# Performance work log

Measured on AMD Instinct MI355X. Metric: run time of the kernel, lower is better.

## Reference

```python
import jax, jax.numpy as jnp
import numpy as np

K = 16          # nsample (ball-query neighbors via topk smallest sqdist)
EPS = 1e-5      # BatchNorm eps


def conv1(x, W, b):
    # pointwise Conv1d (kernel=1): x [B,N,Cin], W [Cout,Cin], b [Cout] -> [B,N,Cout]
    return jnp.einsum('bnc,oc->bno', x, W) + b


def bn_train(x, gamma, beta):
    # BatchNorm1d in training mode: stats over batch and length dims
    mean = jnp.mean(x, axis=(0, 1))
    var = jnp.var(x, axis=(0, 1))
    return (x - mean) * jax.lax.rsqrt(var + EPS) * gamma + beta


def farthest_point_sample(xyz, npoint):
    # xyz [B,N,3] -> idx [B,npoint]; deterministic start at index 0
    B, N, _ = xyz.shape

    def step(carry, _):
        dist, far = carry                                        # [B,N], [B]
        centroid = jnp.take_along_axis(xyz, far[:, None, None], axis=1)  # [B,1,3]
        d = jnp.sum((xyz - centroid) ** 2, axis=-1)              # [B,N]
        dist = jnp.minimum(dist, d)
        nxt = jnp.argmax(dist, axis=1).astype(jnp.int32)
        return (dist, nxt), far

    init = (jnp.full((B, N), jnp.finfo(xyz.dtype).max, xyz.dtype),
            jnp.zeros((B,), jnp.int32))
    _, idx = jax.lax.scan(step, init, None, length=npoint)       # [npoint,B]
    return idx.T                                                  # [B,npoint]


def sqdist(a, b):
    # a [B,S,3], b [B,N,3] -> [B,S,N]
    return (jnp.sum(a ** 2, -1)[:, :, None]
            + jnp.sum(b ** 2, -1)[:, None, :]
            - 2.0 * jnp.einsum('bsc,bnc->bsn', a, b))


def gather_groups(pc, idx):
    # pc [B,N,D], idx [B,S,K] -> [B,S,K,D]
    return jax.vmap(lambda p, i: p[i])(pc, idx)


def setup_inputs() -> dict:
    key = jax.random.key(0)
    ks = jax.random.split(key, 8)
    B, N = 8, 4096
    mid, out, cin = 32, 64, 3
    s = lambda fan: 1.0 / np.sqrt(fan)
    return {
        'x_in': jax.random.normal(ks[0], (B, N, cin), jnp.float32),
        'W1': jax.random.normal(ks[1], (mid, cin), jnp.float32) * s(cin),
        'b1': jnp.zeros((mid,), jnp.float32),
        'g1': jnp.ones((mid,), jnp.float32),
        'be1': jnp.zeros((mid,), jnp.float32),
        'W2': jax.random.normal(ks[2], (out, mid), jnp.float32) * s(mid),
        'b2': jnp.zeros((out,), jnp.float32),
        'W3': jax.random.normal(ks[3], (out, out + cin), jnp.float32) * s(out + cin),
        'b3': jnp.zeros((out,), jnp.float32),
        'g2': jnp.ones((out,), jnp.float32),
        'be2': jnp.zeros((out,), jnp.float32),
        'W4': jax.random.normal(ks[4], (out, out), jnp.float32) * s(out),
        'b4': jnp.zeros((out,), jnp.float32),
    }


def reference(x_in, W1, b1, g1, be1, W2, b2, W3, b3, g2, be2, W4, b4):
    B, N, C = x_in.shape
    S = N // 2
    # first_mlp: Conv1d -> BN -> ReLU -> Conv1d (all pointwise)
    h = jax.nn.relu(bn_train(conv1(x_in, W1, b1), g1, be1))
    feats = conv1(h, W2, b2)                                  # [B,N,64]
    # sample_and_group(npoint=N//2, nsample=K, xyz=x_in, points=feats)
    fps_idx = farthest_point_sample(x_in, S)                  # [B,S]
    new_xyz = jnp.take_along_axis(x_in, fps_idx[..., None], axis=1)  # [B,S,3]
    d = sqdist(new_xyz, x_in)                                 # [B,S,N]
    _, idx = jax.lax.top_k(-d, K)                             # [B,S,K] smallest dists
    grouped_xyz = gather_groups(x_in, idx) - new_xyz[:, :, None, :]  # [B,S,K,3]
    grouped_pts = gather_groups(feats, idx)                   # [B,S,K,64]
    x_cat = jnp.concatenate([grouped_xyz, grouped_pts], axis=-1)  # [B,S,K,67]
    pooled = jnp.max(x_cat, axis=2)                           # [B,S,67]
    # last_mlp
    h = jax.nn.relu(bn_train(conv1(pooled, W3, b3), g2, be2))
    return conv1(h, W4, b4)                                   # [B,S,64]
```

## Files before the change

### kernel.cpp

```cpp
#include <hip/hip_runtime.h>
#include <float.h>

#define BB   8
#define NN   4096
#define SS   2048
#define KK   16
#define MID  32
#define COUT 64
#define CAT  67
#define M1   (BB*NN)
#define M2   (BB*SS)
#define EPSB 1e-5f

#define WS_CTR   0
#define WS_RED1  16
#define WS_RED2  640
#define WS_FPS   1024
#define WS_FEATS (1024 + 16384)
#define WS_POOL  (WS_FEATS + M1*COUT)

struct SA  { float red[8][9]; };
struct SB4 { float4 Pc[NN]; alignas(16) unsigned long long sv[2][8]; };
struct SB3 { float W1s[96]; float abv[64]; float W2s[2048]; float b2s[64]; float mom[9]; };
struct SC  { float4 Pq[NN]; unsigned candd[64][129]; unsigned candi[64][129]; int fin[64][16]; };
struct SC2 { float W3s[64 * CAT]; float b3s[64]; float ps[128]; };
struct SE  { float W3t[CAT * 64]; float W4s[4096]; float b3s[64]; float b4s[64]; float ab[128]; };
union  SU  { SA a; SB4 b4; SB3 b3; SC c; SC2 c2; SE e; };

__device__ __forceinline__ unsigned long long u64max(unsigned long long a,
                                                     unsigned long long b) {
    return a > b ? a : b;
}

template <int CTRL>
__device__ __forceinline__ unsigned long long dpp_swap_max(unsigned long long v) {
    int lo = (int)(unsigned)v;
    int hi = (int)(unsigned)(v >> 32);
    int olo = __builtin_amdgcn_update_dpp(0, lo, CTRL, 0xF, 0xF, false);
    int ohi = __builtin_amdgcn_update_dpp(0, hi, CTRL, 0xF, 0xF, false);
    unsigned long long ov = ((unsigned long long)(unsigned)ohi << 32) | (unsigned)olo;
    return u64max(v, ov);
}

__device__ __forceinline__ void barrier_join(int* ctr, int target) {
    __syncthreads();
    if (threadIdx.x == 0) {
        __threadfence();
        atomicAdd(ctr, 1);
        while (atomicAdd(ctr, 0) < target) __builtin_amdgcn_s_sleep(16);
        __threadfence();
    }
    __syncthreads();
}

__global__ __launch_bounds__(512) void fused(
        const float* __restrict__ xin,
        const float* __restrict__ W1, const float* __restrict__ b1,
        const float* __restrict__ g1, const float* __restrict__ be1,
        const float* __restrict__ W2, const float* __restrict__ b2,
        const float* __restrict__ W3, const float* __restrict__ b3,
        const float* __restrict__ g2, const float* __restrict__ be2,
        const float* __restrict__ W4, const float* __restrict__ b4,
        float* __restrict__ ws, float* __restrict__ out) {
    __shared__ SU sm;
    int blk = blockIdx.x, tid = threadIdx.x;
    int* ctr = (int*)ws;
    (void)b1;

    if (blk >= 8) {
        if (blk < 72) {
            int p = (blk - 8) * 512 + tid;
            float x0 = xin[3 * p], x1 = xin[3 * p + 1], x2 = xin[3 * p + 2];
            float r[9];
            r[0] = x0; r[1] = x1; r[2] = x2;
            r[3] = x0 * x0; r[4] = x0 * x1; r[5] = x0 * x2;
            r[6] = x1 * x1; r[7] = x1 * x2; r[8] = x2 * x2;
#pragma unroll
            for (int m = 32; m; m >>= 1) {
#pragma unroll
                for (int q = 0; q < 9; q++) r[q] += __shfl_down(r[q], m, 64);
            }
            if ((tid & 63) == 0) {
#pragma unroll
                for (int q = 0; q < 9; q++) sm.a.red[tid >> 6][q] = r[q];
            }
            __syncthreads();
            if (tid == 0) {
#pragma unroll
                for (int q = 0; q < 9; q++) {
                    float s = 0.f;
#pragma unroll
                    for (int w = 0; w < 8; w++) s += sm.a.red[w][q];
                    ws[WS_RED1 + (blk - 8) * 9 + q] = s;
                }
            }
        }
        barrier_join(ctr + 0, 248);
    }

    if (blk < 8) {
        int b = blk;
        const float* xb = xin + (size_t)b * NN * 3;
        float px[8], py[8], pz[8], dist[8];
#pragma unroll
        for (int k = 0; k < 8; k++) {
            int i = tid + (k << 9);
            float x = xb[3 * i], y = xb[3 * i + 1], z = xb[3 * i + 2];
            px[k] = x; py[k] = y; pz[k] = z; dist[k] = FLT_MAX;
            sm.b4.Pc[i] = make_float4(x, y, z, 0.f);
        }
        int* fidx = (int*)(ws + WS_FPS) + b * SS;
        if (tid == 0) fidx[0] = 0;
        __syncthreads();
        float4 c0 = sm.b4.Pc[0];
        float cx = c0.x, cy = c0.y, cz = c0.z;
        int wid = tid >> 6, lane = tid & 63;
        for (int t = 1; t < SS; t++) {
            float bv = -1.f; int bi = 0;
#pragma unroll
            for (int k = 0; k < 8; k++) {
                float dx = px[k] - cx, dy = py[k] - cy, dz = pz[k] - cz;
                float d = fmaf(dz, dz, fmaf(dy, dy, dx * dx));
                float nd = fminf(dist[k], d);
                dist[k] = nd;
                bool bt = nd > bv;
                bv = bt ? nd : bv; bi = bt ? (tid + (k << 9)) : bi;
            }
            unsigned long long v =
                ((unsigned long long)__float_as_uint(bv) << 32) | (unsigned)(~bi);
            v = dpp_swap_max<0xB1>(v);
            v = dpp_swap_max<0x4E>(v);
            v = dpp_swap_max<0x141>(v);
            v = dpp_swap_max<0x140>(v);
            {
                int a16 = ((lane ^ 16) << 2), a32 = ((lane ^ 32) << 2), a48 = ((lane ^ 48) << 2);
                int lo = (int)(unsigned)v, hi = (int)(unsigned)(v >> 32);
                int lo16 = __builtin_amdgcn_ds_bpermute(a16, lo);
                int hi16 = __builtin_amdgcn_ds_bpermute(a16, hi);
                int lo32 = __builtin_amdgcn_ds_bpermute(a32, lo);
                int hi32 = __builtin_amdgcn_ds_bpermute(a32, hi);
                int lo48 = __builtin_amdgcn_ds_bpermute(a48, lo);
                int hi48 = __builtin_amdgcn_ds_bpermute(a48, hi);
                unsigned long long v16 = ((unsigned long long)(unsigned)hi16 << 32) | (unsigned)lo16;
                unsigned long long v32 = ((unsigned long long)(unsigned)hi32 << 32) | (unsigned)lo32;
                unsigned long long v48 = ((unsigned long long)(unsigned)hi48 << 32) | (unsigned)lo48;
                v = u64max(u64max(v, v16), u64max(v32, v48));
            }
            int par = t & 1;
            if (lane == 0) sm.b4.sv[par][wid] = v;
            __syncthreads();
            const ulonglong2* sp = (const ulonglong2*)sm.b4.sv[par];
            ulonglong2 q0 = sp[0], q1 = sp[1], q2 = sp[2], q3 = sp[3];
            unsigned long long m0 = u64max(q0.x, q0.y), m1 = u64max(q1.x, q1.y);
            unsigned long long m2 = u64max(q2.x, q2.y), m3 = u64max(q3.x, q3.y);
            unsigned long long best = u64max(u64max(m0, m1), u64max(m2, m3));
            int bsel = (int)(~(unsigned)best);
            float4 cc = sm.b4.Pc[bsel];
            cx = cc.x; cy = cc.y; cz = cc.z;
            if (tid == 0) fidx[t] = bsel;
        }
    } else if (blk < 72) {
        for (int j = tid; j < 96; j += 512) sm.b3.W1s[j] = W1[j];
        if (tid < 64) sm.b3.b2s[tid] = b2[tid];
        for (int j = tid; j < 2048; j += 512) sm.b3.W2s[j] = W2[j];
        if (tid < 9) {
            float s = 0.f;
            for (int k = 0; k < 64; k++) s += ws[WS_RED1 + k * 9 + tid];
            sm.b3.mom[tid] = s;
        }
        __syncthreads();
        if (tid < MID) {
            float S0 = sm.b3.mom[0], S1 = sm.b3.mom[1], S2 = sm.b3.mom[2];
            float C00 = sm.b3.mom[3], C01 = sm.b3.mom[4], C02 = sm.b3.mom[5];
            float C11 = sm.b3.mom[6], C12 = sm.b3.mom[7], C22 = sm.b3.mom[8];
            float w0 = W1[3 * tid], w1 = W1[3 * tid + 1], w2 = W1[3 * tid + 2];
            float invM = 1.f / (float)M1;
            float meanc = (w0 * S0 + w1 * S1 + w2 * S2) * invM;
            float wCw = w0 * w0 * C00 + w1 * w1 * C11 + w2 * w2 * C22 +
                        2.f * (w0 * w1 * C01 + w0 * w2 * C02 + w1 * w2 * C12);
            float var = wCw * invM - meanc * meanc;
            float a = g1[tid] * rsqrtf(var + EPSB);
            sm.b3.abv[tid] = a;
            sm.b3.abv[MID + tid] = be1[tid] - meanc * a;
        }
        __syncthreads();
        int p = (blk - 8) * 512 + tid;
        float x0 = xin[3 * p], x1 = xin[3 * p + 1], x2 = xin[3 * p + 2];
        float h[MID];
#pragma unroll
        for (int o = 0; o < MID; o++) {
            float y = fmaf(sm.b3.W1s[3 * o + 2], x2,
                     fmaf(sm.b3.W1s[3 * o + 1], x1, sm.b3.W1s[3 * o] * x0));
            h[o] = fmaxf(0.f, fmaf(sm.b3.abv[o], y, sm.b3.abv[MID + o]));
        }
        float* fo = ws + WS_FEATS + (size_t)p * COUT;
#pragma unroll
        for (int j = 0; j < COUT; j += 4) {
            float a0 = sm.b3.b2s[j], a1v = sm.b3.b2s[j + 1];
            float a2v = sm.b3.b2s[j + 2], a3v = sm.b3.b2s[j + 3];
#pragma unroll
            for (int o = 0; o < MID; o++) {
                float hv = h[o];
                a0  = fmaf(sm.b3.W2s[(j)     * MID + o], hv, a0);
                a1v = fmaf(sm.b3.W2s[(j + 1) * MID + o], hv, a1v);
                a2v = fmaf(sm.b3.W2s[(j + 2) * MID + o], hv, a2v);
                a3v = fmaf(sm.b3.W2s[(j + 3) * MID + o], hv, a3v);
            }
            *(float4*)(fo + j) = make_float4(a0, a1v, a2v, a3v);
        }
    }
    barrier_join(ctr + 1, 256);

    {
        int b = blk >> 5;
        const float* xb = xin + (size_t)b * NN * 3;
        for (int j = tid; j < NN; j += 512) {
            float x = xb[3 * j], y = xb[3 * j + 1], z = xb[3 * j + 2];
            sm.c.Pq[j] = make_float4(x, y, z, (x * x + y * y) + z * z);
        }
        __syncthreads();
        int cl = tid >> 3, q = tid & 7;
        int sg = blk * 64 + cl;
        const int* fidx = (const int*)(ws + WS_FPS);
        int ci = fidx[sg];
        float4 c = sm.c.Pq[ci];
        float an = c.w;
        unsigned long long cv[16];
#pragma unroll
        for (int j = 0; j < 16; j++) cv[j] = ~0ULL;
        unsigned long long cmaxv = ~0ULL; int cpos = 0;
        for (int n0 = 0; n0 < 512; n0++) {
            int n = (q << 9) + ((n0 + q) & 511);
            float4 qq = sm.c.Pq[n];
            float dot = fmaf(c.z, qq.z, fmaf(c.y, qq.y, c.x * qq.x));
            float dd = (an + qq.w) - 2.f * dot;
            unsigned db = __float_as_uint(dd);
            db ^= (unsigned)(((int)db >> 31) | 0x80000000u);
            unsigned long long newv = ((unsigned long long)db << 32) | (unsigned)n;
            if (newv < cmaxv) {
#pragma unroll
                for (int j = 0; j < 16; j++) cv[j] = (j == cpos) ? newv : cv[j];
                unsigned long long m1a[8]; int p1a[8];
#pragma unroll
                for (int j = 0; j < 8; j++) {
                    bool s = cv[2 * j + 1] > cv[2 * j];
                    m1a[j] = s ? cv[2 * j + 1] : cv[2 * j];
                    p1a[j] = s ? 2 * j + 1 : 2 * j;
                }
                unsigned long long m2a[4]; int p2a[4];
#pragma unroll
                for (int j = 0; j < 4; j++) {
                    bool s = m1a[2 * j + 1] > m1a[2 * j];
                    m2a[j] = s ? m1a[2 * j + 1] : m1a[2 * j];
                    p2a[j] = s ? p1a[2 * j + 1] : p1a[2 * j];
                }
                unsigned long long m3a, m3b; int p3a, p3b;
                { bool s = m2a[1] > m2a[0]; m3a = s ? m2a[1] : m2a[0]; p3a = s ? p2a[1] : p2a[0]; }
                { bool s = m2a[3] > m2a[2]; m3b = s ? m2a[3] : m2a[2]; p3b = s ? p2a[3] : p2a[2]; }
                bool s = m3b > m3a;
                cmaxv = s ? m3b : m3a; cpos = s ? p3b : p3a;
            }
        }
#pragma unroll
        for (int j = 0; j < 16; j++) {
            sm.c.candd[cl][q * 16 + j] = (unsigned)(cv[j] >> 32);
            sm.c.candi[cl][q * 16 + j] = (unsigned)cv[j];
        }
        __syncthreads();
        if (tid < 64) {
            unsigned long long mv[16];
#pragma unroll
            for (int j = 0; j < 16; j++) mv[j] = ~0ULL;
            unsigned long long mx = ~0ULL; int mp = 0;
            for (int k = 0; k < 128; k++) {
                unsigned long long e =
                    ((unsigned long long)sm.c.candd[tid][k] << 32) | sm.c.candi[tid][k];
                if (e < mx) {
#pragma unroll
                    for (int j = 0; j < 16; j++) mv[j] = (j == mp) ? e : mv[j];
                    unsigned long long m1a[8]; int p1a[8];
#pragma unroll
                    for (int j = 0; j < 8; j++) {
                        bool s = mv[2 * j + 1] > mv[2 * j];
                        m1a[j] = s ? mv[2 * j + 1] : mv[2 * j];
                        p1a[j] = s ? 2 * j + 1 : 2 * j;
                    }
                    unsigned long long m2a[4]; int p2a[4];
#pragma unroll
                    for (int j = 0; j < 4; j++) {
                        bool s = m1a[2 * j + 1] > m1a[2 * j];
                        m2a[j] = s ? m1a[2 * j + 1] : m1a[2 * j];
                        p2a[j] = s ? p1a[2 * j + 1] : p1a[2 * j];
                    }
                    unsigned long long m3a, m3b; int p3a, p3b;
                    { bool s = m2a[1] > m2a[0]; m3a = s ? m2a[1] : m2a[0]; p3a = s ? p2a[1] : p2a[0]; }
                    { bool s = m2a[3] > m2a[2]; m3b = s ? m2a[3] : m2a[2]; p3b = s ? p2a[3] : p2a[2]; }
                    bool s = m3b > m3a;
                    mx = s ? m3b : m3a; mp = s ? p3b : p3a;
                }
            }
#pragma unroll
            for (int j = 0; j < 16; j++) sm.c.fin[tid][j] = (int)(unsigned)mv[j];
        }
        __syncthreads();
        int idxs[16];
#pragma unroll
        for (int j = 0; j < 16; j++) idxs[j] = sm.c.fin[cl][j];
        const float* feats = ws + WS_FEATS + (size_t)b * NN * COUT;
        float4 acc0 = make_float4(-FLT_MAX, -FLT_MAX, -FLT_MAX, -FLT_MAX);
        float4 acc1 = acc0;
#pragma unroll 4
        for (int k = 0; k < 16; k++) {
            const float4* fp = (const float4*)(feats + (size_t)idxs[k] * COUT) + q * 2;
            float4 v0 = fp[0], v1 = fp[1];
            acc0.x = fmaxf(acc0.x, v0.x); acc0.y = fmaxf(acc0.y, v0.y);
            acc0.z = fmaxf(acc0.z, v0.z); acc0.w = fmaxf(acc0.w, v0.w);
            acc1.x = fmaxf(acc1.x, v1.x); acc1.y = fmaxf(acc1.y, v1.y);
            acc1.z = fmaxf(acc1.z, v1.z); acc1.w = fmaxf(acc1.w, v1.w);
        }
        float* po = ws + WS_POOL + (size_t)sg * CAT + 3 + q * 8;
        po[0] = acc0.x; po[1] = acc0.y; po[2] = acc0.z; po[3] = acc0.w;
        po[4] = acc1.x; po[5] = acc1.y; po[6] = acc1.z; po[7] = acc1.w;
        if (q == 0) {
            float rx = -FLT_MAX, ry = -FLT_MAX, rz = -FLT_MAX;
#pragma unroll
            for (int k = 0; k < 16; k++) {
                float4 p = sm.c.Pq[idxs[k]];
                rx = fmaxf(rx, p.x - c.x); ry = fmaxf(ry, p.y - c.y); rz = fmaxf(rz, p.z - c.z);
            }
            float* pb = ws + WS_POOL + (size_t)sg * CAT;
            pb[0] = rx; pb[1] = ry; pb[2] = rz;
        }
    }
    barrier_join(ctr + 2, 256);

    if (blk < 64) {
        for (int j = tid; j < 64 * CAT; j += 512) sm.c2.W3s[j] = W3[j];
        if (tid < 64) sm.c2.b3s[tid] = b3[tid];
        if (tid < 128) sm.c2.ps[tid] = 0.f;
        __syncthreads();
        int cch = tid & 63, g = tid >> 6;
        float sum = 0.f, sq = 0.f;
        for (int m = 0; m < 32; m++) {
            int row = blk * 256 + g * 32 + m;
            const float* r = ws + WS_POOL + (size_t)row * CAT;
            float y = sm.c2.b3s[cch];
            for (int j = 0; j < CAT; j++) y = fmaf(sm.c2.W3s[cch * CAT + j], r[j], y);
            sum += y; sq = fmaf(y, y, sq);
        }
        atomicAdd(&sm.c2.ps[cch], sum);
        atomicAdd(&sm.c2.ps[64 + cch], sq);
        __syncthreads();
        if (tid < 128) atomicAdd(ws + WS_RED2 + tid, sm.c2.ps[tid]);
    }
    barrier_join(ctr + 3, 256);

    if (blk < 32) {
        for (int lin = tid; lin < CAT * 64; lin += 512) {
            int j = lin >> 6, o = lin & 63;
            sm.e.W3t[lin] = W3[o * CAT + j];
        }
        for (int j = tid; j < 4096; j += 512) sm.e.W4s[j] = W4[j];
        if (tid < 64) {
            sm.e.b3s[tid] = b3[tid]; sm.e.b4s[tid] = b4[tid];
            float inv = 1.f / (float)M2;
            float mean = ws[WS_RED2 + tid] * inv;
            float var = ws[WS_RED2 + 64 + tid] * inv - mean * mean;
            float a = g2[tid] * rsqrtf(var + EPSB);
            sm.e.ab[tid] = a;
            sm.e.ab[64 + tid] = be2[tid] - mean * a;
        }
        __syncthreads();
        int pt = blk * 512 + tid;
        const float* row = ws + WS_POOL + (size_t)pt * CAT;
        float h[64];
#pragma unroll
        for (int c = 0; c < 64; c++) h[c] = sm.e.b3s[c];
        for (int j = 0; j < CAT; j++) {
            float pj = row[j];
#pragma unroll
            for (int c = 0; c < 64; c++) h[c] = fmaf(sm.e.W3t[j * 64 + c], pj, h[c]);
        }
#pragma unroll
        for (int c = 0; c < 64; c++) h[c] = fmaxf(0.f, fmaf(sm.e.ab[c], h[c], sm.e.ab[64 + c]));
        float* op = out + (size_t)pt * 64;
        for (int o = 0; o < 64; o += 4) {
            float a0 = sm.e.b4s[o], a1v = sm.e.b4s[o + 1];
            float a2v = sm.e.b4s[o + 2], a3v = sm.e.b4s[o + 3];
#pragma unroll
            for (int c = 0; c < 64; c++) {
                float hv = h[c];
                a0  = fmaf(sm.e.W4s[(o)     * 64 + c], hv, a0);
                a1v = fmaf(sm.e.W4s[(o + 1) * 64 + c], hv, a1v);
                a2v = fmaf(sm.e.W4s[(o + 2) * 64 + c], hv, a2v);
                a3v = fmaf(sm.e.W4s[(o + 3) * 64 + c], hv, a3v);
            }
            *(float4*)(op + o) = make_float4(a0, a1v, a2v, a3v);
        }
    }
}

extern "C" void kernel_launch(void* const* d_in, const int* in_sizes, int n_in,
                              void* d_out, int out_size, void* d_ws, size_t ws_size,
                              hipStream_t stream) {
    (void)in_sizes; (void)n_in; (void)out_size; (void)ws_size;
    const float* xin = (const float*)d_in[0];
    const float* W1  = (const float*)d_in[1];
    const float* b1  = (const float*)d_in[2];
    const float* g1  = (const float*)d_in[3];
    const float* be1 = (const float*)d_in[4];
    const float* W2  = (const float*)d_in[5];
    const float* b2  = (const float*)d_in[6];
    const float* W3  = (const float*)d_in[7];
    const float* b3  = (const float*)d_in[8];
    const float* g2  = (const float*)d_in[9];
    const float* be2 = (const float*)d_in[10];
    const float* W4  = (const float*)d_in[11];
    const float* b4  = (const float*)d_in[12];
    float* ws  = (float*)d_ws;
    float* out = (float*)d_out;

    hipMemsetAsync(d_ws, 0, 4096, stream);
    void* args[] = {
        (void*)&xin, (void*)&W1, (void*)&b1, (void*)&g1, (void*)&be1,
        (void*)&W2, (void*)&b2, (void*)&W3, (void*)&b3, (void*)&g2,
        (void*)&be2, (void*)&W4, (void*)&b4, (void*)&ws, (void*)&out
    };
    hipLaunchCooperativeKernel((const void*)fused, dim3(256), dim3(512),
                               args, 0, stream);
}
```

Baseline: 2.361 ms.

## Overlap kNN grouping with FPS via progress flags and dynamic chunk tickets

The farthest-point-sampling blocks now publish their progress every 32 sampled points with release stores. The other 248 blocks compute the first MLP and then pull (batch, chunk) tickets from an atomic counter, spin until that chunk's FPS indices exist, and run top-16 neighbor search and pooling for it. This replaces the old scheme where grouping waited for the whole FPS to finish. The final MLP stages are also spread over all 256 blocks instead of 64 and 32. The cost is spin-wait traffic, reloading the point cloud when a block's batch changes, and the FPS blocks sharing the GPU with the concurrent work.

```diff
diff --git a/kernel.cpp b/kernel.cpp
--- a/kernel.cpp
+++ b/kernel.cpp
@@ -4,17 +4,20 @@
 #define BB   8
 #define NN   4096
 #define SS   2048
-#define KK   16
 #define MID  32
 #define COUT 64
 #define CAT  67
 #define M1   (BB*NN)
 #define M2   (BB*SS)
 #define EPSB 1e-5f
-
-#define WS_CTR   0
-#define WS_RED1  16
-#define WS_RED2  640
+#define NCHUNK 64
+#define CSZ    32
+
+#define WI_CTR   0
+#define WI_TKT   4
+#define WI_PROG  8
+#define WS_RED2  32
+#define WS_RED1  160
 #define WS_FPS   1024
 #define WS_FEATS (1024 + 16384)
 #define WS_POOL  (WS_FEATS + M1*COUT)
@@ -22,7 +25,7 @@
 struct SA  { float red[8][9]; };
 struct SB4 { float4 Pc[NN]; alignas(16) unsigned long long sv[2][8]; };
 struct SB3 { float W1s[96]; float abv[64]; float W2s[2048]; float b2s[64]; float mom[9]; };
-struct SC  { float4 Pq[NN]; unsigned candd[64][129]; unsigned candi[64][129]; int fin[64][16]; };
+struct SC  { float4 Pq[NN]; unsigned long long cand[CSZ][257]; int fin[CSZ][16]; int tkt; };
 struct SC2 { float W3s[64 * CAT]; float b3s[64]; float ps[128]; };
 struct SE  { float W3t[CAT * 64]; float W4s[4096]; float b3s[64]; float b4s[64]; float ab[128]; };
 union  SU  { SA a; SB4 b4; SB3 b3; SC c; SC2 c2; SE e; };
@@ -51,6 +54,32 @@
         __threadfence();
     }
     __syncthreads();
+}
+
+__device__ __forceinline__ void top16_insert(unsigned long long* cv,
+                                             unsigned long long newv,
+                                             unsigned long long& cmaxv, int& cpos) {
+#pragma unroll
+    for (int j = 0; j < 16; j++) cv[j] = (j == cpos) ? newv : cv[j];
+    unsigned long long m1a[8]; int p1a[8];
+#pragma unroll
+    for (int j = 0; j < 8; j++) {
+        bool s = cv[2 * j + 1] > cv[2 * j];
+        m1a[j] = s ? cv[2 * j + 1] : cv[2 * j];
+        p1a[j] = s ? 2 * j + 1 : 2 * j;
+    }
+    unsigned long long m2a[4]; int p2a[4];
+#pragma unroll
+    for (int j = 0; j < 4; j++) {
+        bool s = m1a[2 * j + 1] > m1a[2 * j];
+        m2a[j] = s ? m1a[2 * j + 1] : m1a[2 * j];
+        p2a[j] = s ? p1a[2 * j + 1] : p1a[2 * j];
+    }
+    unsigned long long m3a, m3b; int p3a, p3b;
+    { bool s = m2a[1] > m2a[0]; m3a = s ? m2a[1] : m2a[0]; p3a = s ? p2a[1] : p2a[0]; }
+    { bool s = m2a[3] > m2a[2]; m3b = s ? m2a[3] : m2a[2]; p3b = s ? p2a[3] : p2a[2]; }
+    bool s = m3b > m3a;
+    cmaxv = s ? m3b : m3a; cpos = s ? p3b : p3a;
 }
 
 __global__ __launch_bounds__(512) void fused(
@@ -64,39 +93,10 @@
         float* __restrict__ ws, float* __restrict__ out) {
     __shared__ SU sm;
     int blk = blockIdx.x, tid = threadIdx.x;
-    int* ctr = (int*)ws;
+    int* ctri  = (int*)ws;
+    int* prog  = ctri + WI_PROG;
+    int* fidxg = (int*)(ws + WS_FPS);
     (void)b1;
-
-    if (blk >= 8) {
-        if (blk < 72) {
-            int p = (blk - 8) * 512 + tid;
-            float x0 = xin[3 * p], x1 = xin[3 * p + 1], x2 = xin[3 * p + 2];
-            float r[9];
-            r[0] = x0; r[1] = x1; r[2] = x2;
-            r[3] = x0 * x0; r[4] = x0 * x1; r[5] = x0 * x2;
-            r[6] = x1 * x1; r[7] = x1 * x2; r[8] = x2 * x2;
-#pragma unroll
-            for (int m = 32; m; m >>= 1) {
-#pragma unroll
-                for (int q = 0; q < 9; q++) r[q] += __shfl_down(r[q], m, 64);
-            }
-            if ((tid & 63) == 0) {
-#pragma unroll
-                for (int q = 0; q < 9; q++) sm.a.red[tid >> 6][q] = r[q];
-            }
-            __syncthreads();
-            if (tid == 0) {
-#pragma unroll
-                for (int q = 0; q < 9; q++) {
-                    float s = 0.f;
-#pragma unroll
-                    for (int w = 0; w < 8; w++) s += sm.a.red[w][q];
-                    ws[WS_RED1 + (blk - 8) * 9 + q] = s;
-                }
-            }
-        }
-        barrier_join(ctr + 0, 248);
-    }
 
     if (blk < 8) {
         int b = blk;
@@ -109,8 +109,8 @@
             px[k] = x; py[k] = y; pz[k] = z; dist[k] = FLT_MAX;
             sm.b4.Pc[i] = make_float4(x, y, z, 0.f);
         }
-        int* fidx = (int*)(ws + WS_FPS) + b * SS;
-        if (tid == 0) fidx[0] = 0;
+        if (tid == 0)
+            __hip_atomic_store(fidxg + b * SS, 0, __ATOMIC_RELAXED, __HIP_MEMORY_SCOPE_AGENT);
         __syncthreads();
         float4 c0 = sm.b4.Pc[0];
         float cx = c0.x, cy = c0.y, cz = c0.z;
@@ -157,192 +157,192 @@
             int bsel = (int)(~(unsigned)best);
             float4 cc = sm.b4.Pc[bsel];
             cx = cc.x; cy = cc.y; cz = cc.z;
-            if (tid == 0) fidx[t] = bsel;
-        }
-    } else if (blk < 72) {
-        for (int j = tid; j < 96; j += 512) sm.b3.W1s[j] = W1[j];
-        if (tid < 64) sm.b3.b2s[tid] = b2[tid];
-        for (int j = tid; j < 2048; j += 512) sm.b3.W2s[j] = W2[j];
-        if (tid < 9) {
-            float s = 0.f;
-            for (int k = 0; k < 64; k++) s += ws[WS_RED1 + k * 9 + tid];
-            sm.b3.mom[tid] = s;
-        }
-        __syncthreads();
-        if (tid < MID) {
-            float S0 = sm.b3.mom[0], S1 = sm.b3.mom[1], S2 = sm.b3.mom[2];
-            float C00 = sm.b3.mom[3], C01 = sm.b3.mom[4], C02 = sm.b3.mom[5];
-            float C11 = sm.b3.mom[6], C12 = sm.b3.mom[7], C22 = sm.b3.mom[8];
-            float w0 = W1[3 * tid], w1 = W1[3 * tid + 1], w2 = W1[3 * tid + 2];
-            float invM = 1.f / (float)M1;
-            float meanc = (w0 * S0 + w1 * S1 + w2 * S2) * invM;
-            float wCw = w0 * w0 * C00 + w1 * w1 * C11 + w2 * w2 * C22 +
-                        2.f * (w0 * w1 * C01 + w0 * w2 * C02 + w1 * w2 * C12);
-            float var = wCw * invM - meanc * meanc;
-            float a = g1[tid] * rsqrtf(var + EPSB);
-            sm.b3.abv[tid] = a;
-            sm.b3.abv[MID + tid] = be1[tid] - meanc * a;
-        }
-        __syncthreads();
-        int p = (blk - 8) * 512 + tid;
-        float x0 = xin[3 * p], x1 = xin[3 * p + 1], x2 = xin[3 * p + 2];
-        float h[MID];
-#pragma unroll
-        for (int o = 0; o < MID; o++) {
-            float y = fmaf(sm.b3.W1s[3 * o + 2], x2,
-                     fmaf(sm.b3.W1s[3 * o + 1], x1, sm.b3.W1s[3 * o] * x0));
-            h[o] = fmaxf(0.f, fmaf(sm.b3.abv[o], y, sm.b3.abv[MID + o]));
-        }
-        float* fo = ws + WS_FEATS + (size_t)p * COUT;
-#pragma unroll
-        for (int j = 0; j < COUT; j += 4) {
-            float a0 = sm.b3.b2s[j], a1v = sm.b3.b2s[j + 1];
-            float a2v = sm.b3.b2s[j + 2], a3v = sm.b3.b2s[j + 3];
+            if (tid == 0) {
+                __hip_atomic_store(fidxg + b * SS + t, bsel,
+                                   __ATOMIC_RELAXED, __HIP_MEMORY_SCOPE_AGENT);
+                if (((t + 1) & (CSZ - 1)) == 0)
+                    __hip_atomic_store(prog + b, t + 1,
+                                       __ATOMIC_RELEASE, __HIP_MEMORY_SCOPE_AGENT);
+            }
+        }
+        barrier_join(ctri + 2, 256);
+    } else {
+        if (blk < 72) {
+            int p = (blk - 8) * 512 + tid;
+            float x0 = xin[3 * p], x1 = xin[3 * p + 1], x2 = xin[3 * p + 2];
+            float r[9];
+            r[0] = x0; r[1] = x1; r[2] = x2;
+            r[3] = x0 * x0; r[4] = x0 * x1; r[5] = x0 * x2;
+            r[6] = x1 * x1; r[7] = x1 * x2; r[8] = x2 * x2;
+#pragma unroll
+            for (int m = 32; m; m >>= 1) {
+#pragma unroll
+                for (int q = 0; q < 9; q++) r[q] += __shfl_down(r[q], m, 64);
+            }
+            if ((tid & 63) == 0) {
+#pragma unroll
+                for (int q = 0; q < 9; q++) sm.a.red[tid >> 6][q] = r[q];
+            }
+            __syncthreads();
+            if (tid == 0) {
+#pragma unroll
+                for (int q = 0; q < 9; q++) {
+                    float s = 0.f;
+#pragma unroll
+                    for (int w = 0; w < 8; w++) s += sm.a.red[w][q];
+                    ws[WS_RED1 + (blk - 8) * 9 + q] = s;
+                }
+            }
+            barrier_join(ctri + 0, 64);
+            for (int j = tid; j < 96; j += 512) sm.b3.W1s[j] = W1[j];
+            if (tid < 64) sm.b3.b2s[tid] = b2[tid];
+            for (int j = tid; j < 2048; j += 512) sm.b3.W2s[j] = W2[j];
+            if (tid < 9) {
+                float s = 0.f;
+                for (int k = 0; k < 64; k++) s += ws[WS_RED1 + k * 9 + tid];
+                sm.b3.mom[tid] = s;
+            }
+            __syncthreads();
+            if (tid < MID) {
+                float S0 = sm.b3.mom[0], S1 = sm.b3.mom[1], S2 = sm.b3.mom[2];
+                float C00 = sm.b3.mom[3], C01 = sm.b3.mom[4], C02 = sm.b3.mom[5];
+                float C11 = sm.b3.mom[6], C12 = sm.b3.mom[7], C22 = sm.b3.mom[8];
+                float w0 = W1[3 * tid], w1 = W1[3 * tid + 1], w2 = W1[3 * tid + 2];
+                float invM = 1.f / (float)M1;
+                float meanc = (w0 * S0 + w1 * S1 + w2 * S2) * invM;
+                float wCw = w0 * w0 * C00 + w1 * w1 * C11 + w2 * w2 * C22 +
+                            2.f * (w0 * w1 * C01 + w0 * w2 * C02 + w1 * w2 * C12);
+                float var = wCw * invM - meanc * meanc;
+                float a = g1[tid] * rsqrtf(var + EPSB);
+                sm.b3.abv[tid] = a;
+                sm.b3.abv[MID + tid] = be1[tid] - meanc * a;
+            }
+            __syncthreads();
+            int p2 = (blk - 8) * 512 + tid;
+            float y0 = xin[3 * p2], y1 = xin[3 * p2 + 1], y2 = xin[3 * p2 + 2];
+            float h[MID];
 #pragma unroll
             for (int o = 0; o < MID; o++) {
-                float hv = h[o];
-                a0  = fmaf(sm.b3.W2s[(j)     * MID + o], hv, a0);
-                a1v = fmaf(sm.b3.W2s[(j + 1) * MID + o], hv, a1v);
-                a2v = fmaf(sm.b3.W2s[(j + 2) * MID + o], hv, a2v);
-                a3v = fmaf(sm.b3.W2s[(j + 3) * MID + o], hv, a3v);
-            }
-            *(float4*)(fo + j) = make_float4(a0, a1v, a2v, a3v);
-        }
-    }
-    barrier_join(ctr + 1, 256);
+                float y = fmaf(sm.b3.W1s[3 * o + 2], y2,
+                         fmaf(sm.b3.W1s[3 * o + 1], y1, sm.b3.W1s[3 * o] * y0));
+                h[o] = fmaxf(0.f, fmaf(sm.b3.abv[o], y, sm.b3.abv[MID + o]));
+            }
+            float* fo = ws + WS_FEATS + (size_t)p2 * COUT;
+#pragma unroll
+            for (int j = 0; j < COUT; j += 4) {
+                float a0 = sm.b3.b2s[j], a1v = sm.b3.b2s[j + 1];
+                float a2v = sm.b3.b2s[j + 2], a3v = sm.b3.b2s[j + 3];
+#pragma unroll
+                for (int o = 0; o < MID; o++) {
+                    float hv = h[o];
+                    a0  = fmaf(sm.b3.W2s[(j)     * MID + o], hv, a0);
+                    a1v = fmaf(sm.b3.W2s[(j + 1) * MID + o], hv, a1v);
+                    a2v = fmaf(sm.b3.W2s[(j + 2) * MID + o], hv, a2v);
+                    a3v = fmaf(sm.b3.W2s[(j + 3) * MID + o], hv, a3v);
+                }
+                *(float4*)(fo + j) = make_float4(a0, a1v, a2v, a3v);
+            }
+        }
+        barrier_join(ctri + 1, 248);
+
+        int curb = -1;
+        for (;;) {
+            if (tid == 0) sm.c.tkt = atomicAdd(ctri + WI_TKT, 1);
+            __syncthreads();
+            int tk = sm.c.tkt;
+            if (tk >= BB * NCHUNK) break;
+            int b = tk & 7, c = tk >> 3;
+            if (b != curb) {
+                const float* xb = xin + (size_t)b * NN * 3;
+                for (int j = tid; j < NN; j += 512) {
+                    float x = xb[3 * j], y = xb[3 * j + 1], z = xb[3 * j + 2];
+                    sm.c.Pq[j] = make_float4(x, y, z, (x * x + y * y) + z * z);
+                }
+                curb = b;
+            }
+            if (tid == 0) {
+                int need = (c + 1) * CSZ;
+                while (__hip_atomic_load(prog + b, __ATOMIC_ACQUIRE,
+                                         __HIP_MEMORY_SCOPE_AGENT) < need)
+                    __builtin_amdgcn_s_sleep(8);
+            }
+            __syncthreads();
+            int cc = tid >> 4, q = tid & 15;
+            int s = c * CSZ + cc;
+            int sg = b * SS + s;
+            int ci = __hip_atomic_load(fidxg + sg, __ATOMIC_RELAXED,
+                                       __HIP_MEMORY_SCOPE_AGENT);
+            float4 cen = sm.c.Pq[ci];
+            float an = cen.w;
+            unsigned long long cv[16];
+#pragma unroll
+            for (int j = 0; j < 16; j++) cv[j] = ~0ULL;
+            unsigned long long cmaxv = ~0ULL; int cpos = 0;
+            for (int n0 = 0; n0 < 256; n0++) {
+                int n = (q << 8) + ((n0 + q) & 255);
+                float4 qq = sm.c.Pq[n];
+                float dot = fmaf(cen.z, qq.z, fmaf(cen.y, qq.y, cen.x * qq.x));
+                float dd = (an + qq.w) - 2.f * dot;
+                unsigned db = __float_as_uint(dd);
+                db ^= (unsigned)(((int)db >> 31) | 0x80000000u);
+                unsigned long long newv = ((unsigned long long)db << 32) | (unsigned)n;
+                if (newv < cmaxv) top16_insert(cv, newv, cmaxv, cpos);
+            }
+#pragma unroll
+            for (int j = 0; j < 16; j++) sm.c.cand[cc][q * 16 + j] = cv[j];
+            __syncthreads();
+            if (tid < CSZ) {
+                unsigned long long mv[16];
+#pragma unroll
+                for (int j = 0; j < 16; j++) mv[j] = ~0ULL;
+                unsigned long long mx = ~0ULL; int mp = 0;
+                for (int k = 0; k < 256; k++) {
+                    unsigned long long e = sm.c.cand[tid][k];
+                    if (e < mx) top16_insert(mv, e, mx, mp);
+                }
+#pragma unroll
+                for (int j = 0; j < 16; j++) sm.c.fin[tid][j] = (int)(unsigned)mv[j];
+            }
+            __syncthreads();
+            int idxs[16];
+#pragma unroll
+            for (int j = 0; j < 16; j++) idxs[j] = sm.c.fin[cc][j];
+            const float* feats = ws + WS_FEATS + (size_t)b * NN * COUT;
+            float4 acc = make_float4(-FLT_MAX, -FLT_MAX, -FLT_MAX, -FLT_MAX);
+#pragma unroll 4
+            for (int k = 0; k < 16; k++) {
+                const float4* fp = (const float4*)(feats + (size_t)idxs[k] * COUT) + q;
+                float4 v0 = fp[0];
+                acc.x = fmaxf(acc.x, v0.x); acc.y = fmaxf(acc.y, v0.y);
+                acc.z = fmaxf(acc.z, v0.z); acc.w = fmaxf(acc.w, v0.w);
+            }
+            float* po = ws + WS_POOL + (size_t)sg * CAT;
+            po[3 + q * 4] = acc.x; po[4 + q * 4] = acc.y;
+            po[5 + q * 4] = acc.z; po[6 + q * 4] = acc.w;
+            if (q == 0) {
+                float rx = -FLT_MAX, ry = -FLT_MAX, rz = -FLT_MAX;
+#pragma unroll
+                for (int k = 0; k < 16; k++) {
+                    float4 p = sm.c.Pq[idxs[k]];
+                    rx = fmaxf(rx, p.x - cen.x);
+                    ry = fmaxf(ry, p.y - cen.y);
+                    rz = fmaxf(rz, p.z - cen.z);
+                }
+                po[0] = rx; po[1] = ry; po[2] = rz;
+            }
+        }
+        barrier_join(ctri + 2, 256);
+    }
 
     {
-        int b = blk >> 5;
-        const float* xb = xin + (size_t)b * NN * 3;
-        for (int j = tid; j < NN; j += 512) {
-            float x = xb[3 * j], y = xb[3 * j + 1], z = xb[3 * j + 2];
-            sm.c.Pq[j] = make_float4(x, y, z, (x * x + y * y) + z * z);
-        }
-        __syncthreads();
-        int cl = tid >> 3, q = tid & 7;
-        int sg = blk * 64 + cl;
-        const int* fidx = (const int*)(ws + WS_FPS);
-        int ci = fidx[sg];
-        float4 c = sm.c.Pq[ci];
-        float an = c.w;
-        unsigned long long cv[16];
-#pragma unroll
-        for (int j = 0; j < 16; j++) cv[j] = ~0ULL;
-        unsigned long long cmaxv = ~0ULL; int cpos = 0;
-        for (int n0 = 0; n0 < 512; n0++) {
-            int n = (q << 9) + ((n0 + q) & 511);
-            float4 qq = sm.c.Pq[n];
-            float dot = fmaf(c.z, qq.z, fmaf(c.y, qq.y, c.x * qq.x));
-            float dd = (an + qq.w) - 2.f * dot;
-            unsigned db = __float_as_uint(dd);
-            db ^= (unsigned)(((int)db >> 31) | 0x80000000u);
-            unsigned long long newv = ((unsigned long long)db << 32) | (unsigned)n;
-            if (newv < cmaxv) {
-#pragma unroll
-                for (int j = 0; j < 16; j++) cv[j] = (j == cpos) ? newv : cv[j];
-                unsigned long long m1a[8]; int p1a[8];
-#pragma unroll
-                for (int j = 0; j < 8; j++) {
-                    bool s = cv[2 * j + 1] > cv[2 * j];
-                    m1a[j] = s ? cv[2 * j + 1] : cv[2 * j];
-                    p1a[j] = s ? 2 * j + 1 : 2 * j;
-                }
-                unsigned long long m2a[4]; int p2a[4];
-#pragma unroll
-                for (int j = 0; j < 4; j++) {
-                    bool s = m1a[2 * j + 1] > m1a[2 * j];
-                    m2a[j] = s ? m1a[2 * j + 1] : m1a[2 * j];
-                    p2a[j] = s ? p1a[2 * j + 1] : p1a[2 * j];
-                }
-                unsigned long long m3a, m3b; int p3a, p3b;
-                { bool s = m2a[1] > m2a[0]; m3a = s ? m2a[1] : m2a[0]; p3a = s ? p2a[1] : p2a[0]; }
-                { bool s = m2a[3] > m2a[2]; m3b = s ? m2a[3] : m2a[2]; p3b = s ? p2a[3] : p2a[2]; }
-                bool s = m3b > m3a;
-                cmaxv = s ? m3b : m3a; cpos = s ? p3b : p3a;
-            }
-        }
-#pragma unroll
-        for (int j = 0; j < 16; j++) {
-            sm.c.candd[cl][q * 16 + j] = (unsigned)(cv[j] >> 32);
-            sm.c.candi[cl][q * 16 + j] = (unsigned)cv[j];
-        }
-        __syncthreads();
-        if (tid < 64) {
-            unsigned long long mv[16];
-#pragma unroll
-            for (int j = 0; j < 16; j++) mv[j] = ~0ULL;
-            unsigned long long mx = ~0ULL; int mp = 0;
-            for (int k = 0; k < 128; k++) {
-                unsigned long long e =
-                    ((unsigned long long)sm.c.candd[tid][k] << 32) | sm.c.candi[tid][k];
-                if (e < mx) {
-#pragma unroll
-                    for (int j = 0; j < 16; j++) mv[j] = (j == mp) ? e : mv[j];
-                    unsigned long long m1a[8]; int p1a[8];
-#pragma unroll
-                    for (int j = 0; j < 8; j++) {
-                        bool s = mv[2 * j + 1] > mv[2 * j];
-                        m1a[j] = s ? mv[2 * j + 1] : mv[2 * j];
-                        p1a[j] = s ? 2 * j + 1 : 2 * j;
-                    }
-                    unsigned long long m2a[4]; int p2a[4];
-#pragma unroll
-                    for (int j = 0; j < 4; j++) {
-                        bool s = m1a[2 * j + 1] > m1a[2 * j];
-                        m2a[j] = s ? m1a[2 * j + 1] : m1a[2 * j];
-                        p2a[j] = s ? p1a[2 * j + 1] : p1a[2 * j];
-                    }
-                    unsigned long long m3a, m3b; int p3a, p3b;
-                    { bool s = m2a[1] > m2a[0]; m3a = s ? m2a[1] : m2a[0]; p3a = s ? p2a[1] : p2a[0]; }
-                    { bool s = m2a[3] > m2a[2]; m3b = s ? m2a[3] : m2a[2]; p3b = s ? p2a[3] : p2a[2]; }
-                    bool s = m3b > m3a;
-                    mx = s ? m3b : m3a; mp = s ? p3b : p3a;
-                }
-            }
-#pragma unroll
-            for (int j = 0; j < 16; j++) sm.c.fin[tid][j] = (int)(unsigned)mv[j];
-        }
-        __syncthreads();
-        int idxs[16];
-#pragma unroll
-        for (int j = 0; j < 16; j++) idxs[j] = sm.c.fin[cl][j];
-        const float* feats = ws + WS_FEATS + (size_t)b * NN * COUT;
-        float4 acc0 = make_float4(-FLT_MAX, -FLT_MAX, -FLT_MAX, -FLT_MAX);
-        float4 acc1 = acc0;
-#pragma unroll 4
-        for (int k = 0; k < 16; k++) {
-            const float4* fp = (const float4*)(feats + (size_t)idxs[k] * COUT) + q * 2;
-            float4 v0 = fp[0], v1 = fp[1];
-            acc0.x = fmaxf(acc0.x, v0.x); acc0.y = fmaxf(acc0.y, v0.y);
-            acc0.z = fmaxf(acc0.z, v0.z); acc0.w = fmaxf(acc0.w, v0.w);
-            acc1.x = fmaxf(acc1.x, v1.x); acc1.y = fmaxf(acc1.y, v1.y);
-            acc1.z = fmaxf(acc1.z, v1.z); acc1.w = fmaxf(acc1.w, v1.w);
-        }
-        float* po = ws + WS_POOL + (size_t)sg * CAT + 3 + q * 8;
-        po[0] = acc0.x; po[1] = acc0.y; po[2] = acc0.z; po[3] = acc0.w;
-        po[4] = acc1.x; po[5] = acc1.y; po[6] = acc1.z; po[7] = acc1.w;
-        if (q == 0) {
-            float rx = -FLT_MAX, ry = -FLT_MAX, rz = -FLT_MAX;
-#pragma unroll
-            for (int k = 0; k < 16; k++) {
-                float4 p = sm.c.Pq[idxs[k]];
-                rx = fmaxf(rx, p.x - c.x); ry = fmaxf(ry, p.y - c.y); rz = fmaxf(rz, p.z - c.z);
-            }
-            float* pb = ws + WS_POOL + (size_t)sg * CAT;
-            pb[0] = rx; pb[1] = ry; pb[2] = rz;
-        }
-    }
-    barrier_join(ctr + 2, 256);
-
-    if (blk < 64) {
         for (int j = tid; j < 64 * CAT; j += 512) sm.c2.W3s[j] = W3[j];
         if (tid < 64) sm.c2.b3s[tid] = b3[tid];
         if (tid < 128) sm.c2.ps[tid] = 0.f;
         __syncthreads();
         int cch = tid & 63, g = tid >> 6;
         float sum = 0.f, sq = 0.f;
-        for (int m = 0; m < 32; m++) {
-            int row = blk * 256 + g * 32 + m;
+        for (int m = 0; m < 8; m++) {
+            int row = blk * 64 + g * 8 + m;
             const float* r = ws + WS_POOL + (size_t)row * CAT;
             float y = sm.c2.b3s[cch];
             for (int j = 0; j < CAT; j++) y = fmaf(sm.c2.W3s[cch * CAT + j], r[j], y);
@@ -353,9 +353,9 @@
         __syncthreads();
         if (tid < 128) atomicAdd(ws + WS_RED2 + tid, sm.c2.ps[tid]);
     }
-    barrier_join(ctr + 3, 256);
-
-    if (blk < 32) {
+    barrier_join(ctri + 3, 256);
+
+    {
         for (int lin = tid; lin < CAT * 64; lin += 512) {
             int j = lin >> 6, o = lin & 63;
             sm.e.W3t[lin] = W3[o * CAT + j];
@@ -371,31 +371,34 @@
             sm.e.ab[64 + tid] = be2[tid] - mean * a;
         }
         __syncthreads();
-        int pt = blk * 512 + tid;
-        const float* row = ws + WS_POOL + (size_t)pt * CAT;
-        float h[64];
-#pragma unroll
-        for (int c = 0; c < 64; c++) h[c] = sm.e.b3s[c];
-        for (int j = 0; j < CAT; j++) {
-            float pj = row[j];
-#pragma unroll
-            for (int c = 0; c < 64; c++) h[c] = fmaf(sm.e.W3t[j * 64 + c], pj, h[c]);
-        }
-#pragma unroll
-        for (int c = 0; c < 64; c++) h[c] = fmaxf(0.f, fmaf(sm.e.ab[c], h[c], sm.e.ab[64 + c]));
-        float* op = out + (size_t)pt * 64;
-        for (int o = 0; o < 64; o += 4) {
-            float a0 = sm.e.b4s[o], a1v = sm.e.b4s[o + 1];
-            float a2v = sm.e.b4s[o + 2], a3v = sm.e.b4s[o + 3];
-#pragma unroll
-            for (int c = 0; c < 64; c++) {
-                float hv = h[c];
-                a0  = fmaf(sm.e.W4s[(o)     * 64 + c], hv, a0);
-                a1v = fmaf(sm.e.W4s[(o + 1) * 64 + c], hv, a1v);
-                a2v = fmaf(sm.e.W4s[(o + 2) * 64 + c], hv, a2v);
-                a3v = fmaf(sm.e.W4s[(o + 3) * 64 + c], hv, a3v);
-            }
-            *(float4*)(op + o) = make_float4(a0, a1v, a2v, a3v);
+        if (tid < 64) {
+            int pt = blk * 64 + tid;
+            const float* row = ws + WS_POOL + (size_t)pt * CAT;
+            float h[64];
+#pragma unroll
+            for (int c = 0; c < 64; c++) h[c] = sm.e.b3s[c];
+            for (int j = 0; j < CAT; j++) {
+                float pj = row[j];
+#pragma unroll
+                for (int c = 0; c < 64; c++) h[c] = fmaf(sm.e.W3t[j * 64 + c], pj, h[c]);
+            }
+#pragma unroll
+            for (int c = 0; c < 64; c++)
+                h[c] = fmaxf(0.f, fmaf(sm.e.ab[c], h[c], sm.e.ab[64 + c]));
+            float* op = out + (size_t)pt * 64;
+            for (int o = 0; o < 64; o += 4) {
+                float a0 = sm.e.b4s[o], a1v = sm.e.b4s[o + 1];
+                float a2v = sm.e.b4s[o + 2], a3v = sm.e.b4s[o + 3];
+#pragma unroll
+                for (int c = 0; c < 64; c++) {
+                    float hv = h[c];
+                    a0  = fmaf(sm.e.W4s[(o)     * 64 + c], hv, a0);
+                    a1v = fmaf(sm.e.W4s[(o + 1) * 64 + c], hv, a1v);
+                    a2v = fmaf(sm.e.W4s[(o + 2) * 64 + c], hv, a2v);
+                    a3v = fmaf(sm.e.W4s[(o + 3) * 64 + c], hv, a3v);
+                }
+                *(float4*)(op + o) = make_float4(a0, a1v, a2v, a3v);
+            }
         }
     }
 }
```

Result: faster. 2.182 ms (-7.6%).
